# Kernel optimization log

Measured on AMD Instinct MI355X. Metric: run time of the kernel, lower is better.

Reference implementation:

```python
import jax, jax.numpy as jnp
import numpy as np

_SAMPLING_EPS = 1e-5
BIG_NEG = jnp.float32(-1e30)  # finite stand-in for -inf (exact 0 after softmax in fp32)


def setup_inputs() -> dict:
    key = jax.random.key(0)
    ks = jax.random.split(key, 12)
    B, V, P, O, S = 128, 128000, 2048, 256, 4
    return {
        "logits": jax.random.normal(ks[0], (B, V), jnp.float32) * 4.0,
        "prompt_token_ids": jax.random.randint(ks[1], (B, P), 0, V),
        "output_token_ids": jax.random.randint(ks[2], (B, O), 0, V),
        "stop_token_ids": jax.random.randint(ks[3], (B, S), 0, V),
        "min_tokens": jax.random.randint(ks[4], (B,), 0, 512),
        "presence_penalties": jax.random.uniform(ks[5], (B,), jnp.float32),
        "frequency_penalties": jax.random.uniform(ks[6], (B,), jnp.float32),
        "repetition_penalties": 1.0 + 0.3 * jax.random.uniform(ks[7], (B,), jnp.float32),
        "temperature": 0.5 + jax.random.uniform(ks[8], (B,), jnp.float32),
        "top_k": jax.random.randint(ks[9], (B,), 32, 64),
        "top_p": 0.5 + 0.5 * jax.random.uniform(ks[10], (B,), jnp.float32),
        "uniform_noise": jax.random.uniform(ks[11], (B, V), jnp.float32, minval=1e-10, maxval=1.0),
        "max_num_logprobs": 20,
    }


def reference(logits, prompt_token_ids, output_token_ids, stop_token_ids,
              min_tokens, presence_penalties, frequency_penalties,
              repetition_penalties, temperature, top_k, top_p,
              uniform_noise, max_num_logprobs):
    B, V = logits.shape
    x = logits.astype(jnp.float32)
    rows = jnp.arange(B)[:, None]

    # ---- min-token penalty: set stop-token logits to -inf while len(output) < min_tokens
    need = min_tokens > output_token_ids.shape[1]                  # [B]
    stop_pen = jnp.where(need[:, None], BIG_NEG, jnp.inf)          # [B,S]
    x = x.at[rows, stop_token_ids].min(stop_pen)

    # ---- presence / frequency / repetition penalties (vLLM apply_penalties)
    counts = jnp.zeros((B, V), jnp.float32).at[rows, output_token_ids].add(1.0)
    prompt_mask = jnp.zeros((B, V), bool).at[rows, prompt_token_ids].set(True)
    output_mask = counts > 0
    rp = repetition_penalties[:, None]
    penalized = jnp.where(x > 0, x / rp, x * rp)
    x = jnp.where(prompt_mask | output_mask, penalized, x)
    x = x - frequency_penalties[:, None] * counts \
          - presence_penalties[:, None] * output_mask.astype(jnp.float32)

    # ---- temperature (greedy rows: temp treated as 1.0)
    t = jnp.where(temperature < _SAMPLING_EPS, 1.0, temperature)
    x = x / t[:, None]

    # ---- top-k / top-p filtering (per-row k and p)
    order = jnp.argsort(-x, axis=-1)                               # descending
    srt = jnp.take_along_axis(x, order, axis=-1)
    pos = jnp.arange(V)[None, :]
    k_eff = jnp.where(top_k < 1, V, top_k)
    keep_k = pos < k_eff[:, None]
    probs_s = jax.nn.softmax(srt, axis=-1)
    cum = jnp.cumsum(probs_s, axis=-1)
    keep_p = (cum - probs_s) < top_p[:, None]                      # cumulative mass before token < p
    keep = jnp.zeros((B, V), bool).at[rows, order].set(keep_k & keep_p)
    x = jnp.where(keep, x, BIG_NEG)

    orig_logits = x
    # source applies temperature a second time before the final sample
    x2 = x / t[:, None]

    # ---- sample: Gumbel-max random sampling, greedy where temperature ~ 0
    gumbel = -jnp.log(-jnp.log(uniform_noise))
    random_sampled = jnp.argmax(x2 + gumbel, axis=-1)
    greedy_sampled = jnp.argmax(x2, axis=-1)
    sampled = jnp.where(temperature < _SAMPLING_EPS, greedy_sampled,
                        random_sampled).astype(jnp.int32)

    # ---- top-k logprobs
    logprobs = jax.nn.log_softmax(orig_logits, axis=-1)
    topk_logprobs, topk_indices = jax.lax.top_k(logprobs, max_num_logprobs)
    return sampled, topk_logprobs, topk_indices.astype(jnp.int32)
```

## Files before the change

### kernel.cpp

```cpp
#include <hip/hip_runtime.h>
#include <math.h>

#define VV 128000
#define NB 128
#define PP 2048
#define OO 256
#define GW 4000

#define S   8
#define CH  16000
#define CW  500
#define NT0 512
#define NT1 512
#define CAP 512
#define HS1 512

#define NT2 256

#define BIG_NEG_F (-1e30f)
#define PAD_KEY 0x007FFFFF80000000ULL
#define LOG2E 1.4426950408889634f

__device__ __forceinline__ unsigned long long packkey(float f, int idx) {
  unsigned int b = __float_as_uint(f);
  unsigned int mf = (b & 0x80000000u) ? ~b : (b | 0x80000000u);
  return ((unsigned long long)mf << 32) | (unsigned long long)(unsigned int)(~(unsigned int)idx);
}
__device__ __forceinline__ float unpack_val(unsigned long long k) {
  unsigned int mf = (unsigned int)(k >> 32);
  unsigned int b = (mf & 0x80000000u) ? (mf & 0x7fffffffu) : ~mf;
  return __uint_as_float(b);
}
__device__ __forceinline__ int unpack_idx(unsigned long long k) {
  return (int)(~(unsigned int)(k & 0xffffffffu));
}
__device__ __forceinline__ float ulp_down(float f, int n) {
  unsigned int b = __float_as_uint(f);
  unsigned int m = (b & 0x80000000u) ? ~b : (b | 0x80000000u);
  m -= (unsigned int)n;
  unsigned int r = (m & 0x80000000u) ? (m & 0x7fffffffu) : ~m;
  return __uint_as_float(r);
}

__device__ __forceinline__ float wave_sort64_desc(float v, int lane) {
  for (int k = 2; k <= 64; k <<= 1) {
    for (int j = k >> 1; j > 0; j >>= 1) {
      float o = __shfl_xor(v, j, 64);
      bool smaller = (lane & j) == 0;
      bool dir = (lane & k) == 0;
      v = (smaller == dir) ? fmaxf(v, o) : fminf(v, o);
    }
  }
  return v;
}
__device__ __forceinline__ unsigned long long wave_sort64_desc_u64(unsigned long long v, int lane) {
  for (int k = 2; k <= 64; k <<= 1) {
    for (int j = k >> 1; j > 0; j >>= 1) {
      unsigned long long o = __shfl_xor(v, j, 64);
      bool smaller = (lane & j) == 0;
      bool dir = (lane & k) == 0;
      unsigned long long mx = (v > o) ? v : o;
      unsigned long long mn = (v > o) ? o : v;
      v = (smaller == dir) ? mx : mn;
    }
  }
  return v;
}
__device__ __forceinline__ unsigned long long merge_top64(unsigned long long v,
                                                          const unsigned long long* B,
                                                          int lane) {
  unsigned long long b = B[63 - lane];
  v = (v > b) ? v : b;
  for (int j = 32; j > 0; j >>= 1) {
    unsigned long long o = __shfl_xor(v, j, 64);
    bool hi = (lane & j) == 0;
    unsigned long long mx = (v > o) ? v : o;
    unsigned long long mn = (v > o) ? o : v;
    v = hi ? mx : mn;
  }
  return v;
}

__global__ __launch_bounds__(NT0)
void k0_build(const int* __restrict__ prompt_ids,
              const int* __restrict__ output_ids,
              unsigned int* __restrict__ ws_pb,
              unsigned int* __restrict__ ws_ob,
              int* __restrict__ ws_hk,
              int* __restrict__ ws_hv)
{
  __shared__ int hkey[HS1];
  __shared__ int hval[HS1];
  const int row = blockIdx.x;
  const int tid = threadIdx.x;

  unsigned int* pb = ws_pb + (size_t)row * GW;
  unsigned int* ob = ws_ob + (size_t)row * GW;
  uint4* pb4 = (uint4*)pb;
  uint4* ob4 = (uint4*)ob;
  uint4 z; z.x = 0u; z.y = 0u; z.z = 0u; z.w = 0u;
  for (int i = tid; i < GW / 4; i += NT0) { pb4[i] = z; ob4[i] = z; }
  for (int i = tid; i < HS1; i += NT0) { hkey[i] = -1; hval[i] = 0; }
  __syncthreads();

  const int4* pr4 = (const int4*)(prompt_ids + (size_t)row * PP);
  for (int i = tid; i < PP / 4; i += NT0) {
    int4 tv = pr4[i];
    atomicOr(&pb[tv.x >> 5], 1u << (tv.x & 31));
    atomicOr(&pb[tv.y >> 5], 1u << (tv.y & 31));
    atomicOr(&pb[tv.z >> 5], 1u << (tv.z & 31));
    atomicOr(&pb[tv.w >> 5], 1u << (tv.w & 31));
  }
  for (int i = tid; i < OO; i += NT0) {
    int tok = output_ids[row * OO + i];
    atomicOr(&ob[tok >> 5], 1u << (tok & 31));
    unsigned int h = ((unsigned int)tok * 2654435761u) >> 23;
    for (;;) {
      int k = hkey[h];
      if (k == tok) { atomicAdd(&hval[h], 1); break; }
      if (k == -1) {
        int prev = atomicCAS(&hkey[h], -1, tok);
        if (prev == -1 || prev == tok) { atomicAdd(&hval[h], 1); break; }
        continue;
      }
      h = (h + 1) & (HS1 - 1);
    }
  }
  __syncthreads();
  for (int i = tid; i < HS1; i += NT0) {
    ws_hk[row * HS1 + i] = hkey[i];
    ws_hv[row * HS1 + i] = hval[i];
  }
}

__global__ __launch_bounds__(NT1)
void k1_select(const float* __restrict__ logits,
               const int* __restrict__ stop_ids,
               const int* __restrict__ min_tokens,
               const float* __restrict__ presence_p,
               const float* __restrict__ frequency_p,
               const float* __restrict__ repetition_p,
               const float* __restrict__ temperature,
               const unsigned int* __restrict__ ws_pb,
               const unsigned int* __restrict__ ws_ob,
               const int* __restrict__ ws_hk,
               const int* __restrict__ ws_hv,
               unsigned long long* __restrict__ ws_top,
               float* __restrict__ ws_sum)
{
#pragma clang fp contract(off)
  __shared__ unsigned int pbits[CW];
  __shared__ unsigned int obits[CW];
  __shared__ int hkey[HS1];
  __shared__ int hval[HS1];
  __shared__ unsigned long long cand[CAP];
  __shared__ unsigned long long mbuf[4 * 64];
  __shared__ float wtau[NT1 / 64];
  __shared__ float wsum[NT1 / 64];
  __shared__ float tau_sh;
  __shared__ int cnt_sh;

  const int chunk = blockIdx.x;
  const int row   = blockIdx.y;
  const int tid   = threadIdx.x;
  const int lane  = tid & 63;
  const int wv    = tid >> 6;
  const int base  = chunk * CH;

  const float fp  = frequency_p[row];
  const float pp  = presence_p[row];
  const float rp  = repetition_p[row];
  const float inv_rp = 1.0f / rp;
  const float tmp = temperature[row];
  const float t   = (tmp < 1e-5f) ? 1.0f : tmp;
  const float c2  = LOG2E / t;
  const bool need = min_tokens[row] > OO;
  const int s0 = stop_ids[row * 4 + 0];
  const int s1 = stop_ids[row * 4 + 1];
  const int s2 = stop_ids[row * 4 + 2];
  const int s3 = stop_ids[row * 4 + 3];
  const bool anystop = need &&
      (((unsigned)(s0 - base) < CH) || ((unsigned)(s1 - base) < CH) ||
       ((unsigned)(s2 - base) < CH) || ((unsigned)(s3 - base) < CH));

  const unsigned int* pbg = ws_pb + (size_t)row * GW + chunk * CW;
  const unsigned int* obg = ws_ob + (size_t)row * GW + chunk * CW;
  for (int i = tid; i < CW; i += NT1) { pbits[i] = pbg[i]; obits[i] = obg[i]; }
  for (int i = tid; i < HS1; i += NT1) {
    hkey[i] = ws_hk[row * HS1 + i];
    hval[i] = ws_hv[row * HS1 + i];
  }
  if (tid == 0) cnt_sh = 0;
  __syncthreads();

  const float* __restrict__ lrow = logits + (size_t)row * VV + base;
  const int l0 = (0 * NT1 + tid) << 3;
  const int l1 = (1 * NT1 + tid) << 3;
  const int l2 = (2 * NT1 + tid) << 3;
  const int l3 = (3 * NT1 + tid) << 3;
  const bool v3 = l3 < CH;

  float4 A0 = *(const float4*)(lrow + l0);
  float4 B0 = *(const float4*)(lrow + l0 + 4);
  float4 A1 = *(const float4*)(lrow + l1);
  float4 B1 = *(const float4*)(lrow + l1 + 4);
  float4 A2 = *(const float4*)(lrow + l2);
  float4 B2 = *(const float4*)(lrow + l2 + 4);
  float4 A3, B3;
  if (v3) { A3 = *(const float4*)(lrow + l3); B3 = *(const float4*)(lrow + l3 + 4); }

  float mx = -INFINITY;
  float esum = 0.0f;

  auto processA = [&](int li, float4 xa, float4 xb) {
    unsigned int w  = (unsigned)li >> 5;
    unsigned int sh = (unsigned)li & 31u;
    unsigned int pm8 = (pbits[w] >> sh) & 255u;
    unsigned int om8 = (obits[w] >> sh) & 255u;
    float xs[8] = {xa.x, xa.y, xa.z, xa.w, xb.x, xb.y, xb.z, xb.w};
#pragma unroll
    for (int e = 0; e < 8; ++e) {
      float xp = xs[e];
      int v = base + li + e;
      if (anystop && ((v == s0) | (v == s1) | (v == s2) | (v == s3)))
        xp = BIG_NEG_F;
      if ((pm8 | om8) & (1u << e)) {
        xp = (xp > 0.0f) ? (xp * inv_rp) : (xp * rp);
        if ((om8 >> e) & 1u) {
          float cnt = 0.0f;
          unsigned int h = ((unsigned int)v * 2654435761u) >> 23;
          for (;;) {
            int k = hkey[h];
            if (k == -1) break;
            if (k == v) { cnt = (float)hval[h]; break; }
            h = (h + 1) & (HS1 - 1);
          }
          xp = xp - fp * cnt - pp;
        }
      }
      mx = fmaxf(mx, xp);
      esum += exp2f(xp * c2);
    }
  };

  processA(l0, A0, B0);
  processA(l1, A1, B1);
  processA(l2, A2, B2);
  if (v3) processA(l3, A3, B3);

  float ss = esum;
#pragma unroll
  for (int off = 32; off > 0; off >>= 1) ss += __shfl_down(ss, off, 64);
  if (lane == 0) wsum[wv] = ss;

  float srt = wave_sort64_desc(mx, lane);
  if (lane == 7) wtau[wv] = srt;
  __syncthreads();

  if (tid == 0) {
    float tau = wtau[0];
#pragma unroll
    for (int w = 1; w < NT1 / 64; ++w) tau = fminf(tau, wtau[w]);
    tau_sh = ulp_down(tau, 16);
    float sacc = 0.0f;
#pragma unroll
    for (int w = 0; w < NT1 / 64; ++w) sacc += wsum[w];
    ws_sum[row * S + chunk] = sacc;
  }
  __syncthreads();
  const float taueff = tau_sh;

  A0 = *(const float4*)(lrow + l0); B0 = *(const float4*)(lrow + l0 + 4);
  A1 = *(const float4*)(lrow + l1); B1 = *(const float4*)(lrow + l1 + 4);
  A2 = *(const float4*)(lrow + l2); B2 = *(const float4*)(lrow + l2 + 4);
  if (v3) { A3 = *(const float4*)(lrow + l3); B3 = *(const float4*)(lrow + l3 + 4); }

  auto processB = [&](int li, float4 xa, float4 xb) {
    float xs[8] = {xa.x, xa.y, xa.z, xa.w, xb.x, xb.y, xb.z, xb.w};
#pragma unroll
    for (int e = 0; e < 8; ++e) {
      float x = xs[e];
      if (x >= taueff) {
        int v = base + li + e;
        int ll = li + e;
        if (anystop && ((v == s0) | (v == s1) | (v == s2) | (v == s3)))
          x = fminf(x, BIG_NEG_F);
        bool pm = (pbits[(unsigned)ll >> 5] >> ((unsigned)ll & 31u)) & 1u;
        bool om = (obits[(unsigned)ll >> 5] >> ((unsigned)ll & 31u)) & 1u;
        float cnt = 0.0f;
        if (om) {
          unsigned int h = ((unsigned int)v * 2654435761u) >> 23;
          for (;;) {
            int k = hkey[h];
            if (k == -1) break;
            if (k == v) { cnt = (float)hval[h]; break; }
            h = (h + 1) & (HS1 - 1);
          }
        }
        if (pm || om) x = (x > 0.0f) ? (x / rp) : (x * rp);
        x = x - fp * cnt;
        if (om) x = x - pp;
        if (x >= taueff) {
          float xd = x / t;
          int p = atomicAdd(&cnt_sh, 1);
          if (p < CAP) cand[p] = packkey(xd, v);
        }
      }
    }
  };

  processB(l0, A0, B0);
  processB(l1, A1, B1);
  processB(l2, A2, B2);
  if (v3) processB(l3, A3, B3);

  __syncthreads();
  int total = cnt_sh; if (total > CAP) total = CAP;
  for (int i = tid; i < CAP; i += NT1)
    if (i >= total) cand[i] = PAD_KEY;
  __syncthreads();

  unsigned long long rv = wave_sort64_desc_u64(cand[(wv << 6) + lane], lane);
  cand[(wv << 6) + lane] = rv;
  __syncthreads();

  if (wv < 4) {
    unsigned long long a = cand[((2 * wv) << 6) + lane];
    a = merge_top64(a, &cand[(2 * wv + 1) << 6], lane);
    mbuf[(wv << 6) + lane] = a;
  }
  __syncthreads();
  if (wv < 2) {
    unsigned long long a = mbuf[((2 * wv) << 6) + lane];
    a = merge_top64(a, &mbuf[(2 * wv + 1) << 6], lane);
    cand[(wv << 6) + lane] = a;
  }
  __syncthreads();
  if (wv == 0) {
    unsigned long long a = cand[lane];
    a = merge_top64(a, &cand[64], lane);
    ws_top[((size_t)row * S + chunk) * 64 + lane] = a;
  }
}

__global__ __launch_bounds__(NT2)
void k2_finalize(const float* __restrict__ temperature,
                 const int* __restrict__ top_k,
                 const float* __restrict__ top_p,
                 const float* __restrict__ noise,
                 const unsigned long long* __restrict__ ws_top,
                 const float* __restrict__ ws_sum,
                 float* __restrict__ out, int K)
{
#pragma clang fp contract(off)
  __shared__ unsigned long long buf[S * 64];
  __shared__ unsigned long long mbuf[4 * 64];
  __shared__ float sv[64];
  __shared__ int   si[64];
  __shared__ float se[64];
  __shared__ float gv[64];

  const int row  = blockIdx.x;
  const int tid  = threadIdx.x;
  const int lane = tid & 63;
  const int wv   = tid >> 6;

  const float tmp = temperature[row];
  const float t   = (tmp < 1e-5f) ? 1.0f : tmp;
  const int   tk  = top_k[row];
  const float tpv = top_p[row];

  for (int i = tid; i < S * 64; i += NT2)
    buf[i] = ws_top[(size_t)row * S * 64 + i];
  __syncthreads();

  {
    unsigned long long a = buf[((2 * wv) << 6) + lane];
    a = merge_top64(a, &buf[(2 * wv + 1) << 6], lane);
    mbuf[(wv << 6) + lane] = a;
  }
  __syncthreads();
  if (wv < 2) {
    unsigned long long a = mbuf[((2 * wv) << 6) + lane];
    a = merge_top64(a, &mbuf[(2 * wv + 1) << 6], lane);
    buf[(wv << 6) + lane] = a;
  }
  __syncthreads();
  if (wv == 0) {
    unsigned long long a = buf[lane];
    a = merge_top64(a, &buf[64], lane);
    float val = unpack_val(a);
    int   idx = unpack_idx(a);
    float m = __shfl(val, 0, 64);
    sv[lane] = val;
    si[lane] = idx;
    bool ok = (unsigned)idx < VV;
    float u = ok ? noise[(size_t)row * VV + idx] : 0.5f;
    float g = -logf(-logf(u));
    se[lane] = expf(val - m);
    gv[lane] = val / t + g;
  }
  __syncthreads();

  if (tid == 0) {
    float Ssum = 0.0f;
    for (int c = 0; c < S; c++) Ssum += ws_sum[row * S + c];
    const float m = sv[0];
    const float Z = Ssum * exp2f(-m * LOG2E);

    int keff = (tk < 1) ? 64 : (tk < 64 ? tk : 64);

    float cum = 0.0f;
    int nk = 0;
    for (int j = 0; j < 64; j++) {
      if (j >= keff) break;
      if (!(cum < tpv)) break;
      nk++;
      cum += se[j] / Z;
    }

    float Zk = 0.0f;
    for (int j = 0; j < nk; j++) Zk += se[j];
    const float logZk = logf(Zk);

    float bv = -INFINITY; int bi = 0x7fffffff;
    for (int j = 0; j < nk; j++) {
      float val = gv[j];
      if (val > bv || (val == bv && si[j] < bi)) { bv = val; bi = si[j]; }
    }
    const int samp = (tmp < 1e-5f) ? si[0] : bi;
    out[row] = (float)samp;

    unsigned long long bm0 = 0ull, bm1 = 0ull;
    for (int j = 0; j < nk; j++) {
      int ix = si[j];
      if (ix < 64) bm0 |= 1ull << ix;
      else if (ix < 128) bm1 |= 1ull << (ix - 64);
    }
    int fi = 0;
    for (int j = 0; j < K; j++) {
      float lp; int ix;
      if (j < nk) {
        lp = (sv[j] - m) - logZk;
        ix = si[j];
      } else {
        while ((fi < 64) ? ((bm0 >> fi) & 1ull) : ((bm1 >> (fi - 64)) & 1ull)) fi++;
        ix = fi; fi++;
        lp = BIG_NEG_F;
      }
      out[NB + row * K + j]            = lp;
      out[NB + NB * K + row * K + j]   = (float)ix;
    }
  }
}

extern "C" void kernel_launch(void* const* d_in, const int* in_sizes, int n_in,
                              void* d_out, int out_size, void* d_ws, size_t ws_size,
                              hipStream_t stream) {
  const float* logits = (const float*)d_in[0];
  const int*   prompt = (const int*)d_in[1];
  const int*   outids = (const int*)d_in[2];
  const int*   stop   = (const int*)d_in[3];
  const int*   mint   = (const int*)d_in[4];
  const float* pres   = (const float*)d_in[5];
  const float* freq   = (const float*)d_in[6];
  const float* rep    = (const float*)d_in[7];
  const float* temp   = (const float*)d_in[8];
  const int*   topk   = (const int*)d_in[9];
  const float* topp   = (const float*)d_in[10];
  const float* noise  = (const float*)d_in[11];

  int B_ = in_sizes[4];
  int K_ = (out_size - B_) / (2 * B_);

  unsigned long long* ws_top = (unsigned long long*)d_ws;
  unsigned int* ws_pb = (unsigned int*)(ws_top + (size_t)NB * S * 64);
  unsigned int* ws_ob = ws_pb + (size_t)NB * GW;
  int* ws_hk = (int*)(ws_ob + (size_t)NB * GW);
  int* ws_hv = ws_hk + (size_t)NB * HS1;
  float* ws_sum = (float*)(ws_hv + (size_t)NB * HS1);

  k0_build<<<B_, NT0, 0, stream>>>(prompt, outids, ws_pb, ws_ob, ws_hk, ws_hv);
  dim3 g1(S, B_);
  k1_select<<<g1, NT1, 0, stream>>>(logits, stop, mint, pres, freq, rep, temp,
                                    ws_pb, ws_ob, ws_hk, ws_hv,
                                    ws_top, ws_sum);
  k2_finalize<<<B_, NT2, 0, stream>>>(temp, topk, topp, noise,
                                      ws_top, ws_sum, (float*)d_out, K_);
}
```

Measured before the change: 211.7 us.

## Penalize masked tokens sparsely in build kernel, stream unpenalized chunks through LDS

```diff
diff --git a/kernel.cpp b/kernel.cpp
--- a/kernel.cpp
+++ b/kernel.cpp
@@ -7,19 +7,25 @@
 #define OO 256
 #define GW 4000
 
-#define S   8
-#define CH  16000
-#define CW  500
+#define S    20
+#define CH   6400
+#define CW   200
+#define NSLAB 25
+#define NRUN (S + 1)
+
 #define NT0 512
 #define NT1 512
+#define NT2 256
 #define CAP 512
 #define HS1 512
-
-#define NT2 256
+#define PCAP 2560
 
 #define BIG_NEG_F (-1e30f)
 #define PAD_KEY 0x007FFFFF80000000ULL
 #define LOG2E 1.4426950408889634f
+
+#define AS1(p) ((__attribute__((address_space(1))) void*)(p))
+#define AS3(p) ((__attribute__((address_space(3))) void*)(p))
 
 __device__ __forceinline__ unsigned long long packkey(float f, int idx) {
   unsigned int b = __float_as_uint(f);
@@ -33,13 +39,6 @@
 }
 __device__ __forceinline__ int unpack_idx(unsigned long long k) {
   return (int)(~(unsigned int)(k & 0xffffffffu));
-}
-__device__ __forceinline__ float ulp_down(float f, int n) {
-  unsigned int b = __float_as_uint(f);
-  unsigned int m = (b & 0x80000000u) ? ~b : (b | 0x80000000u);
-  m -= (unsigned int)n;
-  unsigned int r = (m & 0x80000000u) ? (m & 0x7fffffffu) : ~m;
-  return __uint_as_float(r);
 }
 
 __device__ __forceinline__ float wave_sort64_desc(float v, int lane) {
@@ -82,38 +81,62 @@
 }
 
 __global__ __launch_bounds__(NT0)
-void k0_build(const int* __restrict__ prompt_ids,
+void k0_build(const float* __restrict__ logits,
+              const int* __restrict__ prompt_ids,
               const int* __restrict__ output_ids,
-              unsigned int* __restrict__ ws_pb,
-              unsigned int* __restrict__ ws_ob,
-              int* __restrict__ ws_hk,
-              int* __restrict__ ws_hv)
+              const int* __restrict__ stop_ids,
+              const int* __restrict__ min_tokens,
+              const float* __restrict__ presence_p,
+              const float* __restrict__ frequency_p,
+              const float* __restrict__ repetition_p,
+              const float* __restrict__ temperature,
+              unsigned int* __restrict__ ws_mb,
+              unsigned long long* __restrict__ ws_top,
+              float* __restrict__ ws_sum)
 {
+#pragma clang fp contract(off)
+  __shared__ unsigned int pobits[GW];
   __shared__ int hkey[HS1];
   __shared__ int hval[HS1];
+  __shared__ __align__(16) unsigned long long penk[PCAP];
+  __shared__ unsigned long long cand[CAP];
+  __shared__ float wtau[NT0 / 64];
+  __shared__ float wsum[NT0 / 64];
+  __shared__ float tau_sh;
+  __shared__ int pcnt_sh, cnt_sh;
+
   const int row = blockIdx.x;
   const int tid = threadIdx.x;
-
-  unsigned int* pb = ws_pb + (size_t)row * GW;
-  unsigned int* ob = ws_ob + (size_t)row * GW;
-  uint4* pb4 = (uint4*)pb;
-  uint4* ob4 = (uint4*)ob;
-  uint4 z; z.x = 0u; z.y = 0u; z.z = 0u; z.w = 0u;
-  for (int i = tid; i < GW / 4; i += NT0) { pb4[i] = z; ob4[i] = z; }
+  const int lane = tid & 63;
+  const int wv = tid >> 6;
+
+  const float fp = frequency_p[row];
+  const float pp = presence_p[row];
+  const float rp = repetition_p[row];
+  const float tmp = temperature[row];
+  const float t = (tmp < 1e-5f) ? 1.0f : tmp;
+  const bool need = min_tokens[row] > OO;
+  const int s0 = stop_ids[row * 4 + 0], s1 = stop_ids[row * 4 + 1],
+            s2 = stop_ids[row * 4 + 2], s3 = stop_ids[row * 4 + 3];
+
+  { uint4 z; z.x = z.y = z.z = z.w = 0u;
+    uint4* pb4 = (uint4*)pobits;
+    for (int i = tid; i < GW / 4; i += NT0) pb4[i] = z; }
   for (int i = tid; i < HS1; i += NT0) { hkey[i] = -1; hval[i] = 0; }
-  __syncthreads();
-
-  const int4* pr4 = (const int4*)(prompt_ids + (size_t)row * PP);
-  for (int i = tid; i < PP / 4; i += NT0) {
-    int4 tv = pr4[i];
-    atomicOr(&pb[tv.x >> 5], 1u << (tv.x & 31));
-    atomicOr(&pb[tv.y >> 5], 1u << (tv.y & 31));
-    atomicOr(&pb[tv.z >> 5], 1u << (tv.z & 31));
-    atomicOr(&pb[tv.w >> 5], 1u << (tv.w & 31));
-  }
+  if (tid == 0) { pcnt_sh = 0; cnt_sh = 0; }
+  __syncthreads();
+
+  { const int4* pr4 = (const int4*)(prompt_ids + (size_t)row * PP);
+    for (int i = tid; i < PP / 4; i += NT0) {
+      int4 tv = pr4[i];
+      atomicOr(&pobits[tv.x >> 5], 1u << (tv.x & 31));
+      atomicOr(&pobits[tv.y >> 5], 1u << (tv.y & 31));
+      atomicOr(&pobits[tv.z >> 5], 1u << (tv.z & 31));
+      atomicOr(&pobits[tv.w >> 5], 1u << (tv.w & 31));
+    } }
   for (int i = tid; i < OO; i += NT0) {
     int tok = output_ids[row * OO + i];
-    atomicOr(&ob[tok >> 5], 1u << (tok & 31));
+    atomicOr(&pobits[tok >> 5], 1u << (tok & 31));
     unsigned int h = ((unsigned int)tok * 2654435761u) >> 23;
     for (;;) {
       int k = hkey[h];
@@ -127,219 +150,212 @@
     }
   }
   __syncthreads();
-  for (int i = tid; i < HS1; i += NT0) {
-    ws_hk[row * HS1 + i] = hkey[i];
-    ws_hv[row * HS1 + i] = hval[i];
+
+  float penmax = -INFINITY;
+  float esum = 0.0f;
+  for (int w = tid; w < GW; w += NT0) {
+    unsigned pb = pobits[w];
+    unsigned sw = 0u;
+    if (need) {
+      if ((s0 >> 5) == w) sw |= 1u << (s0 & 31);
+      if ((s1 >> 5) == w) sw |= 1u << (s1 & 31);
+      if ((s2 >> 5) == w) sw |= 1u << (s2 & 31);
+      if ((s3 >> 5) == w) sw |= 1u << (s3 & 31);
+    }
+    unsigned mw = pb | sw;
+    ws_mb[(size_t)row * GW + w] = mw;
+    while (mw) {
+      int b = __ffs(mw) - 1;
+      mw &= mw - 1;
+      int tok = (w << 5) + b;
+      float x = logits[(size_t)row * VV + tok];
+      if (need && (tok == s0 || tok == s1 || tok == s2 || tok == s3))
+        x = fminf(x, BIG_NEG_F);
+      bool pmom = (pb >> b) & 1u;
+      float cnt = 0.0f;
+      { unsigned int h = ((unsigned int)tok * 2654435761u) >> 23;
+        for (;;) {
+          int k = hkey[h];
+          if (k == -1) break;
+          if (k == tok) { cnt = (float)hval[h]; break; }
+          h = (h + 1) & (HS1 - 1);
+        } }
+      bool om = cnt > 0.0f;
+      if (pmom) x = (x > 0.0f) ? (x / rp) : (x * rp);
+      x = x - fp * cnt;
+      if (om) x = x - pp;
+      float xd = x / t;
+      esum += exp2f(xd * LOG2E);
+      penmax = fmaxf(penmax, xd);
+      int p = atomicAdd(&pcnt_sh, 1);
+      if (p < PCAP) penk[p] = packkey(xd, tok);
+    }
+  }
+
+  float ssr = esum;
+  for (int off = 32; off > 0; off >>= 1) ssr += __shfl_down(ssr, off, 64);
+  if (lane == 0) wsum[wv] = ssr;
+  float srt = wave_sort64_desc(penmax, lane);
+  if (lane == 7) wtau[wv] = srt;
+  __syncthreads();
+  if (tid == 0) {
+    float tau = wtau[0];
+    for (int w2 = 1; w2 < NT0 / 64; ++w2) tau = fminf(tau, wtau[w2]);
+    tau_sh = tau;
+    float sa = 0.0f;
+    for (int w2 = 0; w2 < NT0 / 64; ++w2) sa += wsum[w2];
+    ws_sum[row * NRUN + S] = sa;
+  }
+  __syncthreads();
+
+  const unsigned long long thr = packkey(tau_sh, 0x7fffffff);
+  int np = pcnt_sh; if (np > PCAP) np = PCAP;
+  for (int i = tid; i < np; i += NT0) {
+    unsigned long long k = penk[i];
+    if (k >= thr) { int p = atomicAdd(&cnt_sh, 1); if (p < CAP) cand[p] = k; }
+  }
+  __syncthreads();
+  int total = cnt_sh; if (total > CAP) total = CAP;
+  for (int i = tid; i < CAP; i += NT0) if (i >= total) cand[i] = PAD_KEY;
+  __syncthreads();
+  unsigned long long rv = wave_sort64_desc_u64(cand[(wv << 6) + lane], lane);
+  cand[(wv << 6) + lane] = rv;
+  __syncthreads();
+  unsigned long long* mb = penk;
+  if (wv < 4) {
+    unsigned long long a = cand[((2 * wv) << 6) + lane];
+    a = merge_top64(a, &cand[(2 * wv + 1) << 6], lane);
+    mb[(wv << 6) + lane] = a;
+  }
+  __syncthreads();
+  if (wv < 2) {
+    unsigned long long a = mb[((2 * wv) << 6) + lane];
+    a = merge_top64(a, &mb[(2 * wv + 1) << 6], lane);
+    cand[(wv << 6) + lane] = a;
+  }
+  __syncthreads();
+  if (wv == 0) {
+    unsigned long long a = cand[lane];
+    a = merge_top64(a, &cand[64], lane);
+    ws_top[((size_t)row * NRUN + S) * 64 + lane] = a;
   }
 }
 
 __global__ __launch_bounds__(NT1)
 void k1_select(const float* __restrict__ logits,
-               const int* __restrict__ stop_ids,
-               const int* __restrict__ min_tokens,
-               const float* __restrict__ presence_p,
-               const float* __restrict__ frequency_p,
-               const float* __restrict__ repetition_p,
                const float* __restrict__ temperature,
-               const unsigned int* __restrict__ ws_pb,
-               const unsigned int* __restrict__ ws_ob,
-               const int* __restrict__ ws_hk,
-               const int* __restrict__ ws_hv,
+               const unsigned int* __restrict__ ws_mb,
                unsigned long long* __restrict__ ws_top,
                float* __restrict__ ws_sum)
 {
-#pragma clang fp contract(off)
-  __shared__ unsigned int pbits[CW];
-  __shared__ unsigned int obits[CW];
-  __shared__ int hkey[HS1];
-  __shared__ int hval[HS1];
+  __shared__ __align__(16) float chbuf[CH];
+  __shared__ unsigned int mbits[CW];
   __shared__ unsigned long long cand[CAP];
-  __shared__ unsigned long long mbuf[4 * 64];
   __shared__ float wtau[NT1 / 64];
   __shared__ float wsum[NT1 / 64];
   __shared__ float tau_sh;
   __shared__ int cnt_sh;
 
-  const int chunk = blockIdx.x;
-  const int row   = blockIdx.y;
-  const int tid   = threadIdx.x;
-  const int lane  = tid & 63;
-  const int wv    = tid >> 6;
-  const int base  = chunk * CH;
-
-  const float fp  = frequency_p[row];
-  const float pp  = presence_p[row];
-  const float rp  = repetition_p[row];
-  const float inv_rp = 1.0f / rp;
+  const int ck  = blockIdx.x;
+  const int row = blockIdx.y;
+  const int tid = threadIdx.x;
+  const int lane = tid & 63;
+  const int wv = tid >> 6;
+  const int base = ck * CH;
+
   const float tmp = temperature[row];
-  const float t   = (tmp < 1e-5f) ? 1.0f : tmp;
-  const float c2  = LOG2E / t;
-  const bool need = min_tokens[row] > OO;
-  const int s0 = stop_ids[row * 4 + 0];
-  const int s1 = stop_ids[row * 4 + 1];
-  const int s2 = stop_ids[row * 4 + 2];
-  const int s3 = stop_ids[row * 4 + 3];
-  const bool anystop = need &&
-      (((unsigned)(s0 - base) < CH) || ((unsigned)(s1 - base) < CH) ||
-       ((unsigned)(s2 - base) < CH) || ((unsigned)(s3 - base) < CH));
-
-  const unsigned int* pbg = ws_pb + (size_t)row * GW + chunk * CW;
-  const unsigned int* obg = ws_ob + (size_t)row * GW + chunk * CW;
-  for (int i = tid; i < CW; i += NT1) { pbits[i] = pbg[i]; obits[i] = obg[i]; }
-  for (int i = tid; i < HS1; i += NT1) {
-    hkey[i] = ws_hk[row * HS1 + i];
-    hval[i] = ws_hv[row * HS1 + i];
-  }
+  const float t = (tmp < 1e-5f) ? 1.0f : tmp;
+  const float c2 = LOG2E / t;
+
+  const float* lrow = logits + (size_t)row * VV + base;
+  for (int slab = wv; slab < NSLAB; slab += NT1 / 64) {
+    __builtin_amdgcn_global_load_lds(AS1(lrow + (slab << 8) + (lane << 2)),
+                                     AS3(chbuf + (slab << 8)), 16, 0, 0);
+  }
+  { const uint4* src = (const uint4*)(ws_mb + (size_t)row * GW + ck * CW);
+    if (tid < CW / 4) ((uint4*)mbits)[tid] = src[tid]; }
   if (tid == 0) cnt_sh = 0;
   __syncthreads();
-
-  const float* __restrict__ lrow = logits + (size_t)row * VV + base;
-  const int l0 = (0 * NT1 + tid) << 3;
-  const int l1 = (1 * NT1 + tid) << 3;
-  const int l2 = (2 * NT1 + tid) << 3;
-  const int l3 = (3 * NT1 + tid) << 3;
-  const bool v3 = l3 < CH;
-
-  float4 A0 = *(const float4*)(lrow + l0);
-  float4 B0 = *(const float4*)(lrow + l0 + 4);
-  float4 A1 = *(const float4*)(lrow + l1);
-  float4 B1 = *(const float4*)(lrow + l1 + 4);
-  float4 A2 = *(const float4*)(lrow + l2);
-  float4 B2 = *(const float4*)(lrow + l2 + 4);
-  float4 A3, B3;
-  if (v3) { A3 = *(const float4*)(lrow + l3); B3 = *(const float4*)(lrow + l3 + 4); }
 
   float mx = -INFINITY;
   float esum = 0.0f;
-
-  auto processA = [&](int li, float4 xa, float4 xb) {
-    unsigned int w  = (unsigned)li >> 5;
-    unsigned int sh = (unsigned)li & 31u;
-    unsigned int pm8 = (pbits[w] >> sh) & 255u;
-    unsigned int om8 = (obits[w] >> sh) & 255u;
-    float xs[8] = {xa.x, xa.y, xa.z, xa.w, xb.x, xb.y, xb.z, xb.w};
+  const float4* ch4 = (const float4*)chbuf;
 #pragma unroll
-    for (int e = 0; e < 8; ++e) {
-      float xp = xs[e];
-      int v = base + li + e;
-      if (anystop && ((v == s0) | (v == s1) | (v == s2) | (v == s3)))
-        xp = BIG_NEG_F;
-      if ((pm8 | om8) & (1u << e)) {
-        xp = (xp > 0.0f) ? (xp * inv_rp) : (xp * rp);
-        if ((om8 >> e) & 1u) {
-          float cnt = 0.0f;
-          unsigned int h = ((unsigned int)v * 2654435761u) >> 23;
-          for (;;) {
-            int k = hkey[h];
-            if (k == -1) break;
-            if (k == v) { cnt = (float)hval[h]; break; }
-            h = (h + 1) & (HS1 - 1);
-          }
-          xp = xp - fp * cnt - pp;
+  for (int it = 0; it < 4; ++it) {
+    int i4 = it * NT1 + tid;
+    if (i4 < CH / 4) {
+      float4 xv = ch4[i4];
+      unsigned mw = mbits[i4 >> 3];
+      unsigned m4 = (mw >> ((i4 & 7) << 2)) & 15u;
+#pragma unroll
+      for (int e = 0; e < 4; ++e) {
+        float x = (&xv.x)[e];
+        float xm = (m4 & (1u << e)) ? -INFINITY : x;
+        mx = fmaxf(mx, xm);
+        esum += exp2f(xm * c2);
+      }
+    }
+  }
+
+  float ssr = esum;
+  for (int off = 32; off > 0; off >>= 1) ssr += __shfl_down(ssr, off, 64);
+  if (lane == 0) wsum[wv] = ssr;
+  float srt = wave_sort64_desc(mx, lane);
+  if (lane == 7) wtau[wv] = srt;
+  __syncthreads();
+  if (tid == 0) {
+    float tau = wtau[0];
+    for (int w = 1; w < NT1 / 64; ++w) tau = fminf(tau, wtau[w]);
+    tau_sh = tau;
+    float sa = 0.0f;
+    for (int w = 0; w < NT1 / 64; ++w) sa += wsum[w];
+    ws_sum[row * NRUN + ck] = sa;
+  }
+  __syncthreads();
+  const float taueff = tau_sh;
+
+#pragma unroll
+  for (int it = 0; it < 4; ++it) {
+    int i4 = it * NT1 + tid;
+    if (i4 < CH / 4) {
+      float4 xv = ch4[i4];
+      unsigned mw = mbits[i4 >> 3];
+      unsigned m4 = (mw >> ((i4 & 7) << 2)) & 15u;
+#pragma unroll
+      for (int e = 0; e < 4; ++e) {
+        float x = (&xv.x)[e];
+        if (x >= taueff && !(m4 & (1u << e))) {
+          int p = atomicAdd(&cnt_sh, 1);
+          if (p < CAP) cand[p] = packkey(x / t, base + (i4 << 2) + e);
         }
       }
-      mx = fmaxf(mx, xp);
-      esum += exp2f(xp * c2);
-    }
-  };
-
-  processA(l0, A0, B0);
-  processA(l1, A1, B1);
-  processA(l2, A2, B2);
-  if (v3) processA(l3, A3, B3);
-
-  float ss = esum;
-#pragma unroll
-  for (int off = 32; off > 0; off >>= 1) ss += __shfl_down(ss, off, 64);
-  if (lane == 0) wsum[wv] = ss;
-
-  float srt = wave_sort64_desc(mx, lane);
-  if (lane == 7) wtau[wv] = srt;
-  __syncthreads();
-
-  if (tid == 0) {
-    float tau = wtau[0];
-#pragma unroll
-    for (int w = 1; w < NT1 / 64; ++w) tau = fminf(tau, wtau[w]);
-    tau_sh = ulp_down(tau, 16);
-    float sacc = 0.0f;
-#pragma unroll
-    for (int w = 0; w < NT1 / 64; ++w) sacc += wsum[w];
-    ws_sum[row * S + chunk] = sacc;
-  }
-  __syncthreads();
-  const float taueff = tau_sh;
-
-  A0 = *(const float4*)(lrow + l0); B0 = *(const float4*)(lrow + l0 + 4);
-  A1 = *(const float4*)(lrow + l1); B1 = *(const float4*)(lrow + l1 + 4);
-  A2 = *(const float4*)(lrow + l2); B2 = *(const float4*)(lrow + l2 + 4);
-  if (v3) { A3 = *(const float4*)(lrow + l3); B3 = *(const float4*)(lrow + l3 + 4); }
-
-  auto processB = [&](int li, float4 xa, float4 xb) {
-    float xs[8] = {xa.x, xa.y, xa.z, xa.w, xb.x, xb.y, xb.z, xb.w};
-#pragma unroll
-    for (int e = 0; e < 8; ++e) {
-      float x = xs[e];
-      if (x >= taueff) {
-        int v = base + li + e;
-        int ll = li + e;
-        if (anystop && ((v == s0) | (v == s1) | (v == s2) | (v == s3)))
-          x = fminf(x, BIG_NEG_F);
-        bool pm = (pbits[(unsigned)ll >> 5] >> ((unsigned)ll & 31u)) & 1u;
-        bool om = (obits[(unsigned)ll >> 5] >> ((unsigned)ll & 31u)) & 1u;
-        float cnt = 0.0f;
-        if (om) {
-          unsigned int h = ((unsigned int)v * 2654435761u) >> 23;
-          for (;;) {
-            int k = hkey[h];
-            if (k == -1) break;
-            if (k == v) { cnt = (float)hval[h]; break; }
-            h = (h + 1) & (HS1 - 1);
-          }
-        }
-        if (pm || om) x = (x > 0.0f) ? (x / rp) : (x * rp);
-        x = x - fp * cnt;
-        if (om) x = x - pp;
-        if (x >= taueff) {
-          float xd = x / t;
-          int p = atomicAdd(&cnt_sh, 1);
-          if (p < CAP) cand[p] = packkey(xd, v);
-        }
-      }
-    }
-  };
-
-  processB(l0, A0, B0);
-  processB(l1, A1, B1);
-  processB(l2, A2, B2);
-  if (v3) processB(l3, A3, B3);
-
+    }
+  }
   __syncthreads();
   int total = cnt_sh; if (total > CAP) total = CAP;
-  for (int i = tid; i < CAP; i += NT1)
-    if (i >= total) cand[i] = PAD_KEY;
+  for (int i = tid; i < CAP; i += NT1) if (i >= total) cand[i] = PAD_KEY;
   __syncthreads();
 
   unsigned long long rv = wave_sort64_desc_u64(cand[(wv << 6) + lane], lane);
   cand[(wv << 6) + lane] = rv;
   __syncthreads();
-
+  unsigned long long* mb = (unsigned long long*)chbuf;
   if (wv < 4) {
     unsigned long long a = cand[((2 * wv) << 6) + lane];
     a = merge_top64(a, &cand[(2 * wv + 1) << 6], lane);
-    mbuf[(wv << 6) + lane] = a;
+    mb[(wv << 6) + lane] = a;
   }
   __syncthreads();
   if (wv < 2) {
-    unsigned long long a = mbuf[((2 * wv) << 6) + lane];
-    a = merge_top64(a, &mbuf[(2 * wv + 1) << 6], lane);
+    unsigned long long a = mb[((2 * wv) << 6) + lane];
+    a = merge_top64(a, &mb[(2 * wv + 1) << 6], lane);
     cand[(wv << 6) + lane] = a;
   }
   __syncthreads();
   if (wv == 0) {
     unsigned long long a = cand[lane];
     a = merge_top64(a, &cand[64], lane);
-    ws_top[((size_t)row * S + chunk) * 64 + lane] = a;
+    ws_top[((size_t)row * NRUN + ck) * 64 + lane] = a;
   }
 }
 
@@ -353,44 +369,45 @@
                  float* __restrict__ out, int K)
 {
 #pragma clang fp contract(off)
-  __shared__ unsigned long long buf[S * 64];
-  __shared__ unsigned long long mbuf[4 * 64];
+  __shared__ unsigned long long runs[32 * 64];
+  __shared__ unsigned long long scr[16 * 64];
   __shared__ float sv[64];
   __shared__ int   si[64];
   __shared__ float se[64];
   __shared__ float gv[64];
 
-  const int row  = blockIdx.x;
-  const int tid  = threadIdx.x;
+  const int row = blockIdx.x;
+  const int tid = threadIdx.x;
   const int lane = tid & 63;
-  const int wv   = tid >> 6;
+  const int wv = tid >> 6;
 
   const float tmp = temperature[row];
-  const float t   = (tmp < 1e-5f) ? 1.0f : tmp;
-  const int   tk  = top_k[row];
+  const float t = (tmp < 1e-5f) ? 1.0f : tmp;
+  const int tk = top_k[row];
   const float tpv = top_p[row];
 
-  for (int i = tid; i < S * 64; i += NT2)
-    buf[i] = ws_top[(size_t)row * S * 64 + i];
-  __syncthreads();
-
-  {
-    unsigned long long a = buf[((2 * wv) << 6) + lane];
-    a = merge_top64(a, &buf[(2 * wv + 1) << 6], lane);
-    mbuf[(wv << 6) + lane] = a;
-  }
-  __syncthreads();
-  if (wv < 2) {
-    unsigned long long a = mbuf[((2 * wv) << 6) + lane];
-    a = merge_top64(a, &mbuf[(2 * wv + 1) << 6], lane);
-    buf[(wv << 6) + lane] = a;
-  }
-  __syncthreads();
+  for (int i = tid; i < 32 * 64; i += NT2) {
+    int r = i >> 6;
+    runs[i] = (r < NRUN) ? ws_top[((size_t)row * NRUN + r) * 64 + (i & 63)]
+                         : PAD_KEY;
+  }
+  __syncthreads();
+
+  unsigned long long* p = runs;
+  unsigned long long* q = scr;
+  for (int nout = 16; nout >= 1; nout >>= 1) {
+    for (int m = wv; m < nout; m += 4) {
+      unsigned long long a = p[((2 * m) << 6) + lane];
+      a = merge_top64(a, &p[((2 * m + 1) << 6)], lane);
+      q[(m << 6) + lane] = a;
+    }
+    __syncthreads();
+    unsigned long long* tp = p; p = q; q = tp;
+  }
   if (wv == 0) {
-    unsigned long long a = buf[lane];
-    a = merge_top64(a, &buf[64], lane);
+    unsigned long long a = p[lane];
     float val = unpack_val(a);
-    int   idx = unpack_idx(a);
+    int idx = unpack_idx(a);
     float m = __shfl(val, 0, 64);
     sv[lane] = val;
     si[lane] = idx;
@@ -404,7 +421,7 @@
 
   if (tid == 0) {
     float Ssum = 0.0f;
-    for (int c = 0; c < S; c++) Ssum += ws_sum[row * S + c];
+    for (int c = 0; c < NRUN; c++) Ssum += ws_sum[row * NRUN + c];
     const float m = sv[0];
     const float Z = Ssum * exp2f(-m * LOG2E);
 
@@ -474,17 +491,14 @@
   int K_ = (out_size - B_) / (2 * B_);
 
   unsigned long long* ws_top = (unsigned long long*)d_ws;
-  unsigned int* ws_pb = (unsigned int*)(ws_top + (size_t)NB * S * 64);
-  unsigned int* ws_ob = ws_pb + (size_t)NB * GW;
-  int* ws_hk = (int*)(ws_ob + (size_t)NB * GW);
-  int* ws_hv = ws_hk + (size_t)NB * HS1;
-  float* ws_sum = (float*)(ws_hv + (size_t)NB * HS1);
-
-  k0_build<<<B_, NT0, 0, stream>>>(prompt, outids, ws_pb, ws_ob, ws_hk, ws_hv);
+  unsigned int* ws_mb = (unsigned int*)(ws_top + (size_t)NB * NRUN * 64);
+  float* ws_sum = (float*)(ws_mb + (size_t)NB * GW);
+
+  k0_build<<<B_, NT0, 0, stream>>>(logits, prompt, outids, stop, mint,
+                                   pres, freq, rep, temp,
+                                   ws_mb, ws_top, ws_sum);
   dim3 g1(S, B_);
-  k1_select<<<g1, NT1, 0, stream>>>(logits, stop, mint, pres, freq, rep, temp,
-                                    ws_pb, ws_ob, ws_hk, ws_hv,
-                                    ws_top, ws_sum);
+  k1_select<<<g1, NT1, 0, stream>>>(logits, temp, ws_mb, ws_top, ws_sum);
   k2_finalize<<<B_, NT2, 0, stream>>>(temp, topk, topp, noise,
                                       ws_top, ws_sum, (float*)d_out, K_);
 }
```

Result: slower. 253.7 us (+19.8%).
